# Kernel optimization log

Hardware: AMD Instinct MI355X
Metric: run time of the kernel (lower is better)

The kernel has to match this reference:

```python
import jax, jax.numpy as jnp
import numpy as np

N = 4096
F_IN = 512
ALPHA = 0.2          # LeakyReLU negative slope
NEG_INF = -9e15      # mask fill used by pyGAT


def setup_inputs() -> dict:
    key = jax.random.key(0)
    ks = jax.random.split(key, 9)
    x = jax.random.normal(ks[0], (N, F_IN), dtype=jnp.float32)
    adj = (jax.random.uniform(ks[1], (N, N)) < 0.005).astype(jnp.float32)
    adj = jnp.maximum(adj, jnp.eye(N, dtype=jnp.float32))
    s = 0.05
    W1 = jax.random.normal(ks[2], (512, 8, 128), dtype=jnp.float32) * s
    a_src1 = jax.random.normal(ks[3], (8, 128), dtype=jnp.float32) * s
    a_dst1 = jax.random.normal(ks[4], (8, 128), dtype=jnp.float32) * s
    W2 = jax.random.normal(ks[5], (1024, 1, 16), dtype=jnp.float32) * s
    a_src2 = jax.random.normal(ks[6], (1, 16), dtype=jnp.float32) * s
    a_dst2 = jax.random.normal(ks[7], (1, 16), dtype=jnp.float32) * s
    return {"x": x, "adj": adj, "W1": W1, "a_src1": a_src1, "a_dst1": a_dst1,
            "W2": W2, "a_src2": a_src2, "a_dst2": a_dst2}


def gat_layer(x, mask, W, a_src, a_dst, concat, activation):
    # x: [N, Fin], W: [Fin, H, Fout]
    h = jnp.einsum('nf,fho->nho', x, W)                  # [N, H, Fout]
    f_src = jnp.einsum('nho,ho->hn', h, a_src)            # [H, N]
    f_dst = jnp.einsum('nho,ho->hn', h, a_dst)            # [H, N]
    e = f_src[:, :, None] + f_dst[:, None, :]             # [H, N, N]
    e = jax.nn.leaky_relu(e, ALPHA)
    e = jnp.where(mask[None, :, :], e, NEG_INF)
    attn = jax.nn.softmax(e, axis=-1)                     # masked softmax over neighbors j
    out = jnp.einsum('hij,jho->iho', attn, h)             # [N, H, Fout]
    if concat:
        out = out.reshape(out.shape[0], -1)               # [N, H*Fout]
    else:
        out = out.mean(axis=1)                            # [N, Fout]
    if activation:
        out = jax.nn.elu(out)
    return out


def reference(x, adj, W1, a_src1, a_dst1, W2, a_src2, a_dst2):
    mask = adj > 0
    h1 = gat_layer(x, mask, W1, a_src1, a_dst1, concat=True, activation=True)
    h2 = gat_layer(h1, mask, W2, a_src2, a_dst2, concat=False, activation=False)
    out = jax.nn.elu(h2)
    return jax.nn.log_softmax(out, axis=1)
```

## Files before the change

### kernel.cpp

```cpp
#include <hip/hip_runtime.h>
#include <hip/hip_bf16.h>
#include <hip/hip_fp16.h>

typedef __attribute__((ext_vector_type(8))) short short8;
typedef __attribute__((ext_vector_type(8))) _Float16 half8;
typedef __attribute__((ext_vector_type(2))) _Float16 h2v;
typedef __attribute__((ext_vector_type(4))) float f32x4;
typedef __attribute__((ext_vector_type(2))) float f32x2;

#define MAXNBR 128
#define ALPHA 0.2f

static __device__ __forceinline__ unsigned short f2h(float f) {
    return __half_as_ushort(__float2half(f));
}
static __device__ __forceinline__ float h2f(unsigned short u) {
    return __half2float(__ushort_as_half(u));
}

__global__ __launch_bounds__(256) void cvt(const float* __restrict__ x,
                                           unsigned short* __restrict__ xh,
                                           const float* __restrict__ W1,
                                           unsigned short* __restrict__ W1t) {
    __shared__ float tile[64][65];
    int b = blockIdx.x, t = threadIdx.x;
    if (b < 1024) {
        size_t base = (size_t)b * 2048 + t * 8;
        float4 v0 = *(const float4*)&x[base];
        float4 v1 = *(const float4*)&x[base + 4];
        short8 o;
        o[0] = f2h(v0.x); o[1] = f2h(v0.y); o[2] = f2h(v0.z); o[3] = f2h(v0.w);
        o[4] = f2h(v1.x); o[5] = f2h(v1.y); o[6] = f2h(v1.z); o[7] = f2h(v1.w);
        *(short8*)&xh[base] = o;
    } else {
        int tb = b - 1024;
        int tk = (tb >> 4) * 64, tc = (tb & 15) * 64;
        int g = t >> 6, cx = t & 63;
        #pragma unroll
        for (int r = 0; r < 16; ++r)
            tile[g * 16 + r][cx] = W1[(size_t)(tk + g * 16 + r) * 1024 + tc + cx];
        __syncthreads();
        #pragma unroll
        for (int r = 0; r < 16; ++r)
            W1t[(size_t)(tc + g * 16 + r) * 512 + tk + cx] = f2h(tile[cx][g * 16 + r]);
    }
}

__global__ __launch_bounds__(256) void gemm_scan(const unsigned short* __restrict__ A,
                                                 const unsigned short* __restrict__ Bt,
                                                 unsigned short* __restrict__ C,
                                                 const float* __restrict__ adj,
                                                 int* __restrict__ nbr_idx,
                                                 int* __restrict__ nbr_cnt) {
    __shared__ unsigned short Asm[128 * 64];
    __shared__ unsigned short Bsm[64 * 64];
    __shared__ int wsum[4];
    int b = blockIdx.x;
    int tid = threadIdx.x;
    if (b < 512) {
        int lane = tid & 63;
        int w = tid >> 6;
        int wr = w >> 1, wc = w & 1;
        int rowBase = (b & 31) * 128, colBase = (b >> 5) * 64;
        int lr = lane >> 3;
        int lcs = ((lane & 7) ^ lr) * 8;
        f32x4 acc[4][2] = {};
        for (int k0 = 0; k0 < 512; k0 += 64) {
            #pragma unroll
            for (int i = 0; i < 4; ++i) {
                int rA = i * 32 + w * 8;
                __builtin_amdgcn_global_load_lds(
                    (const __attribute__((address_space(1))) void*)&A[(size_t)(rowBase + rA + lr) * 512 + k0 + lcs],
                    (__attribute__((address_space(3))) void*)&Asm[rA * 64],
                    16, 0, 0);
            }
            #pragma unroll
            for (int i = 0; i < 2; ++i) {
                int rB = i * 32 + w * 8;
                __builtin_amdgcn_global_load_lds(
                    (const __attribute__((address_space(1))) void*)&Bt[(size_t)(colBase + rB + lr) * 512 + k0 + lcs],
                    (__attribute__((address_space(3))) void*)&Bsm[rB * 64],
                    16, 0, 0);
            }
            __syncthreads();
            #pragma unroll
            for (int kk = 0; kk < 64; kk += 32) {
                half8 af[4], bfv[2];
                int kf = kk + (lane >> 4) * 8;
                #pragma unroll
                for (int m = 0; m < 4; ++m) {
                    int R = wr * 64 + m * 16 + (lane & 15);
                    af[m] = *(const half8*)&Asm[R * 64 + (kf ^ ((R & 7) << 3))];
                }
                #pragma unroll
                for (int n = 0; n < 2; ++n) {
                    int R = wc * 32 + n * 16 + (lane & 15);
                    bfv[n] = *(const half8*)&Bsm[R * 64 + (kf ^ ((R & 7) << 3))];
                }
                #pragma unroll
                for (int m = 0; m < 4; ++m)
                    #pragma unroll
                    for (int n = 0; n < 2; ++n)
                        acc[m][n] = __builtin_amdgcn_mfma_f32_16x16x32_f16(af[m], bfv[n], acc[m][n], 0, 0, 0);
            }
            __syncthreads();
        }
        int crow0 = rowBase + wr * 64, ccol0 = colBase + wc * 32;
        #pragma unroll
        for (int m = 0; m < 4; ++m)
            #pragma unroll
            for (int n = 0; n < 2; ++n) {
                int col = ccol0 + n * 16 + (lane & 15);
                int row0 = crow0 + m * 16 + (lane >> 4) * 4;
                #pragma unroll
                for (int r = 0; r < 4; ++r)
                    C[(size_t)(row0 + r) * 1024 + col] = f2h(acc[m][n][r]);
            }
    } else {
        int row = b - 512;
        int t = tid;
        const float* arow = adj + (size_t)row * 4096;
        const float4* ap = (const float4*)(arow + t * 16);
        float4 v0 = ap[0], v1 = ap[1], v2 = ap[2], v3 = ap[3];
        unsigned mask = 0;
        #pragma unroll
        for (int q = 0; q < 4; ++q) {
            if (((const float*)&v0)[q] > 0.f) mask |= 1u << q;
            if (((const float*)&v1)[q] > 0.f) mask |= 1u << (4 + q);
            if (((const float*)&v2)[q] > 0.f) mask |= 1u << (8 + q);
            if (((const float*)&v3)[q] > 0.f) mask |= 1u << (12 + q);
        }
        int mycnt = __popc(mask);
        int lane = t & 63, w = t >> 6;
        int incl = mycnt;
        #pragma unroll
        for (int d = 1; d < 64; d <<= 1) {
            int nn = __shfl_up(incl, d);
            if (lane >= d) incl += nn;
        }
        if (lane == 63) wsum[w] = incl;
        __syncthreads();
        int base = (w > 0 ? wsum[0] : 0) + (w > 1 ? wsum[1] : 0) + (w > 2 ? wsum[2] : 0);
        int pos = base + incl - mycnt;
        #pragma unroll
        for (int q = 0; q < 16; ++q) {
            if (mask & (1u << q)) {
                if (pos < MAXNBR) nbr_idx[row * MAXNBR + pos] = t * 16 + q;
                ++pos;
            }
        }
        if (t == 255) {
            int tot = base + incl;
            nbr_cnt[row] = tot < MAXNBR ? tot : MAXNBR;
        }
    }
}

__global__ __launch_bounds__(256) void attn_coef1(const unsigned short* __restrict__ h1h,
                                                  const float* __restrict__ a_src,
                                                  const float* __restrict__ a_dst,
                                                  float* __restrict__ fsp,
                                                  float* __restrict__ fdp,
                                                  unsigned char* __restrict__ h1q) {
    int n = blockIdx.x, t = threadIdx.x;
    ushort4 v = *(const ushort4*)&h1h[(size_t)n * 1024 + t * 4];
    int head = t >> 5;
    int o0 = (t * 4) & 127;
    float hv0 = h2f(v.x), hv1 = h2f(v.y), hv2 = h2f(v.z), hv3 = h2f(v.w);
    {
        int w8 = __builtin_amdgcn_cvt_pk_fp8_f32(hv0, hv1, 0, false);
        w8 = __builtin_amdgcn_cvt_pk_fp8_f32(hv2, hv3, w8, true);
        *(unsigned*)&h1q[(size_t)n * 1024 + t * 4] = (unsigned)w8;
    }
    float ps = hv0 * a_src[head * 128 + o0] + hv1 * a_src[head * 128 + o0 + 1]
             + hv2 * a_src[head * 128 + o0 + 2] + hv3 * a_src[head * 128 + o0 + 3];
    float pd = hv0 * a_dst[head * 128 + o0] + hv1 * a_dst[head * 128 + o0 + 1]
             + hv2 * a_dst[head * 128 + o0 + 2] + hv3 * a_dst[head * 128 + o0 + 3];
    #pragma unroll
    for (int off = 1; off < 32; off <<= 1) {
        ps += __shfl_xor(ps, off);
        pd += __shfl_xor(pd, off);
    }
    if ((t & 31) == 0) {
        fsp[n * 8 + head] = ps;
        fdp[n * 8 + head] = pd;
    }
}

__global__ __launch_bounds__(512) void aggregate7(const unsigned char* __restrict__ h1q,
                                                  const int* __restrict__ nbr_idx,
                                                  const int* __restrict__ nbr_cnt,
                                                  const float* __restrict__ fsp,
                                                  const float* __restrict__ fdp,
                                                  unsigned short* __restrict__ h1act) {
    __shared__ int nbr[MAXNBR];
    __shared__ float e_s[8][MAXNBR];
    __shared__ _Float16 attwS[8][MAXNBR];
    __shared__ half8 partS[3][128];
    int i = blockIdx.x;
    int t = threadIdx.x;
    int cnt = nbr_cnt[i];
    if (t < MAXNBR) {
        int nb = (t < cnt) ? nbr_idx[i * MAXNBR + t] : 0;
        nbr[t] = nb;
        if (t < cnt) {
            float4 fs0 = *(const float4*)&fsp[i * 8];
            float4 fs1 = *(const float4*)&fsp[i * 8 + 4];
            float4 d0 = *(const float4*)&fdp[nb * 8];
            float4 d1 = *(const float4*)&fdp[nb * 8 + 4];
            float e0 = fs0.x + d0.x, e1 = fs0.y + d0.y, e2 = fs0.z + d0.z, e3 = fs0.w + d0.w;
            float e4 = fs1.x + d1.x, e5 = fs1.y + d1.y, e6 = fs1.z + d1.z, e7 = fs1.w + d1.w;
            e_s[0][t] = e0 > 0.f ? e0 : ALPHA * e0;
            e_s[1][t] = e1 > 0.f ? e1 : ALPHA * e1;
            e_s[2][t] = e2 > 0.f ? e2 : ALPHA * e2;
            e_s[3][t] = e3 > 0.f ? e3 : ALPHA * e3;
            e_s[4][t] = e4 > 0.f ? e4 : ALPHA * e4;
            e_s[5][t] = e5 > 0.f ? e5 : ALPHA * e5;
            e_s[6][t] = e6 > 0.f ? e6 : ALPHA * e6;
            e_s[7][t] = e7 > 0.f ? e7 : ALPHA * e7;
        } else {
            #pragma unroll
            for (int h = 0; h < 8; ++h) e_s[h][t] = -INFINITY;
        }
    }
    __syncthreads();
    if (t < 256) {
        int h = t >> 5, sl = t & 31;
        float e[4];
        #pragma unroll
        for (int p = 0; p < 4; ++p) e[p] = e_s[h][sl + p * 32];
        float m = fmaxf(fmaxf(e[0], e[1]), fmaxf(e[2], e[3]));
        #pragma unroll
        for (int off = 1; off < 32; off <<= 1) m = fmaxf(m, __shfl_xor(m, off));
        float wq[4], s = 0.f;
        #pragma unroll
        for (int p = 0; p < 4; ++p) {
            wq[p] = (e[p] == -INFINITY) ? 0.f : __expf(e[p] - m);
            s += wq[p];
        }
        #pragma unroll
        for (int off = 1; off < 32; off <<= 1) s += __shfl_xor(s, off);
        float inv = 1.f / s;
        #pragma unroll
        for (int p = 0; p < 4; ++p)
            attwS[h][sl + p * 32] = (_Float16)(wq[p] * inv);
    }
    __syncthreads();
    int tf = t & 127;
    int par = t >> 7;
    int head = tf >> 4;
    const unsigned char* src = h1q + tf * 8;
    float acc[8] = {0.f, 0.f, 0.f, 0.f, 0.f, 0.f, 0.f, 0.f};
    int cntPad = (cnt + 3) & ~3;
    for (int j = par; j < cntPad; j += 4) {
        int nb = nbr[j];
        float wv = (float)attwS[head][j];
        uint2 v = *(const uint2*)&src[(size_t)nb << 10];
        f32x2 p0 = __builtin_amdgcn_cvt_pk_f32_fp8((int)v.x, false);
        f32x2 p1 = __builtin_amdgcn_cvt_pk_f32_fp8((int)v.x, true);
        f32x2 p2 = __builtin_amdgcn_cvt_pk_f32_fp8((int)v.y, false);
        f32x2 p3 = __builtin_amdgcn_cvt_pk_f32_fp8((int)v.y, true);
        acc[0] += wv * p0[0]; acc[1] += wv * p0[1];
        acc[2] += wv * p1[0]; acc[3] += wv * p1[1];
        acc[4] += wv * p2[0]; acc[5] += wv * p2[1];
        acc[6] += wv * p3[0]; acc[7] += wv * p3[1];
    }
    if (par > 0) {
        half8 st;
        #pragma unroll
        for (int q = 0; q < 8; ++q) st[q] = (_Float16)acc[q];
        partS[par - 1][tf] = st;
    }
    __syncthreads();
    if (par == 0) {
        half8 p0 = partS[0][tf], p1 = partS[1][tf], p2 = partS[2][tf];
        short8 o;
        #pragma unroll
        for (int q = 0; q < 8; ++q) {
            float a = acc[q] + (float)p0[q] + (float)p1[q] + (float)p2[q];
            a = a > 0.f ? a : (__expf(a) - 1.f);
            o[q] = f2h(a);
        }
        *(short8*)&h1act[(size_t)i * 1024 + tf * 8] = o;
    }
}

__global__ __launch_bounds__(256) void layer2_mfma(const unsigned short* __restrict__ h1act,
                                                   const float* __restrict__ W2,
                                                   const float* __restrict__ a_src2,
                                                   const float* __restrict__ a_dst2,
                                                   float* __restrict__ h2,
                                                   float2* __restrict__ fsd2) {
    __shared__ unsigned short W2t[16 * 1032];
    __shared__ float pred[4][256];
    int t = threadIdx.x, lane = t & 63, w = t >> 6;
    int rowBase = blockIdx.x * 16;
    for (int idx = t; idx < 16384; idx += 256) {
        int k = idx >> 4, o = idx & 15;
        W2t[o * 1032 + k] = f2h(W2[idx]);
    }
    __syncthreads();
    f32x4 acc = {};
    int r0 = lane & 15, kg = (lane >> 4) * 8;
    #pragma unroll
    for (int kk = 0; kk < 256; kk += 32) {
        int k0 = w * 256 + kk;
        half8 af = *(const half8*)&h1act[(size_t)(rowBase + r0) * 1024 + k0 + kg];
        half8 bf = *(const half8*)&W2t[r0 * 1032 + k0 + kg];
        acc = __builtin_amdgcn_mfma_f32_16x16x32_f16(af, bf, acc, 0, 0, 0);
    }
    #pragma unroll
    for (int r = 0; r < 4; ++r)
        pred[w][((lane >> 4) * 4 + r) * 16 + (lane & 15)] = acc[r];
    __syncthreads();
    if (t < 256) {
        int row = t >> 4, col = t & 15;
        float s = pred[0][t] + pred[1][t] + pred[2][t] + pred[3][t];
        h2[(rowBase + row) * 16 + col] = s;
        float ps = s * a_src2[col];
        float pd = s * a_dst2[col];
        #pragma unroll
        for (int off = 1; off < 16; off <<= 1) {
            ps += __shfl_xor(ps, off);
            pd += __shfl_xor(pd, off);
        }
        if (col == 0) fsd2[rowBase + row] = make_float2(ps, pd);
    }
}

__global__ __launch_bounds__(64) void final_layer(const float* __restrict__ h2,
                                                  const int* __restrict__ nbr_idx,
                                                  const int* __restrict__ nbr_cnt,
                                                  const float2* __restrict__ fsd2,
                                                  float* __restrict__ out) {
    __shared__ float attn[MAXNBR];
    __shared__ int nbr[MAXNBR];
    int i = blockIdx.x;
    int l = threadIdx.x;
    int cnt = nbr_cnt[i];
    float fsi = fsd2[i].x;
    for (int j = l; j < MAXNBR; j += 64) {
        float e = -INFINITY;
        if (j < cnt) {
            int jj = nbr_idx[i * MAXNBR + j];
            nbr[j] = jj;
            float xv = fsi + fsd2[jj].y;
            e = xv > 0.f ? xv : ALPHA * xv;
        }
        attn[j] = e;
    }
    __syncthreads();
    float m = fmaxf(attn[l], attn[l + 64]);
    #pragma unroll
    for (int off = 1; off < 64; off <<= 1) m = fmaxf(m, __shfl_xor(m, off));
    float s = 0.f;
    {
        float e0 = attn[l], e1 = attn[l + 64];
        if (e0 != -INFINITY) s += __expf(e0 - m);
        if (e1 != -INFINITY) s += __expf(e1 - m);
    }
    #pragma unroll
    for (int off = 1; off < 64; off <<= 1) s += __shfl_xor(s, off);
    for (int j = l; j < MAXNBR; j += 64) {
        float e = attn[j];
        attn[j] = (e == -INFINITY) ? 0.f : __expf(e - m) / s;
    }
    __syncthreads();
    if (l < 16) {
        float acc = 0.f;
        for (int j = 0; j < cnt; ++j)
            acc += attn[j] * h2[nbr[j] * 16 + l];
        float v = acc > 0.f ? acc : expm1f(acc);
        float mx = v;
        #pragma unroll
        for (int off = 1; off < 16; off <<= 1) mx = fmaxf(mx, __shfl_xor(mx, off));
        float se = __expf(v - mx);
        #pragma unroll
        for (int off = 1; off < 16; off <<= 1) se += __shfl_xor(se, off);
        out[i * 16 + l] = v - mx - logf(se);
    }
}

extern "C" void kernel_launch(void* const* d_in, const int* in_sizes, int n_in,
                              void* d_out, int out_size, void* d_ws, size_t ws_size,
                              hipStream_t stream) {
    const float* x      = (const float*)d_in[0];
    const float* adj    = (const float*)d_in[1];
    const float* W1     = (const float*)d_in[2];
    const float* a_src1 = (const float*)d_in[3];
    const float* a_dst1 = (const float*)d_in[4];
    const float* W2     = (const float*)d_in[5];
    const float* a_src2 = (const float*)d_in[6];
    const float* a_dst2 = (const float*)d_in[7];
    float* out = (float*)d_out;

    char* ws = (char*)d_ws;
    unsigned short* xh    = (unsigned short*)ws;
    unsigned short* w1t   = (unsigned short*)(ws + (4u << 20));
    unsigned short* h1h   = (unsigned short*)(ws + (6u << 20));
    float* fsp   = (float*)(ws + (14u << 20));
    float* fdp   = (float*)(ws + (14u << 20) + (128u << 10));
    float* h2    = (float*)(ws + (15u << 20));
    float2* fsd2 = (float2*)(ws + (15u << 20) + (256u << 10));
    int* nbr_idx = (int*)(ws + (16u << 20));
    int* nbr_cnt = (int*)(ws + (18u << 20));
    unsigned short* h1act = (unsigned short*)(ws + (26u << 20));
    unsigned char* h1q    = (unsigned char*)(ws + (34u << 20));

    cvt<<<1152, 256, 0, stream>>>(x, xh, W1, w1t);
    gemm_scan<<<4608, 256, 0, stream>>>(xh, w1t, h1h, adj, nbr_idx, nbr_cnt);
    attn_coef1<<<4096, 256, 0, stream>>>(h1h, a_src1, a_dst1, fsp, fdp, h1q);
    aggregate7<<<4096, 512, 0, stream>>>(h1q, nbr_idx, nbr_cnt, fsp, fdp, h1act);
    layer2_mfma<<<256, 256, 0, stream>>>(h1act, W2, a_src2, a_dst2, h2, fsd2);
    final_layer<<<4096, 64, 0, stream>>>(h2, nbr_idx, nbr_cnt, fsd2, out);
}
```

Measured before the change: 65.22 us.

## Fuse fp8 quantization into GEMM epilogue and pack multiple nodes per block

The GEMM epilogue now writes the fp8 copy of h1 directly, so the coefficient kernel no longer produces h1q and only computes the attention projections, with one wave per node and four nodes per block. The aggregation kernel handles two nodes per 512-thread block, each with 256 threads in two partitions instead of four. The final layer packs four nodes per block, drops its block barriers because each wave owns its own shared slices, and splits the neighbor sum across all 64 lanes. This cuts block count and launch overhead, but the epilogue now does scattered per-byte fp8 stores, which may be poorly coalesced.

```diff
diff --git a/kernel.cpp b/kernel.cpp
--- a/kernel.cpp
+++ b/kernel.cpp
@@ -4,7 +4,6 @@
 
 typedef __attribute__((ext_vector_type(8))) short short8;
 typedef __attribute__((ext_vector_type(8))) _Float16 half8;
-typedef __attribute__((ext_vector_type(2))) _Float16 h2v;
 typedef __attribute__((ext_vector_type(4))) float f32x4;
 typedef __attribute__((ext_vector_type(2))) float f32x2;
 
@@ -49,6 +48,7 @@
 __global__ __launch_bounds__(256) void gemm_scan(const unsigned short* __restrict__ A,
                                                  const unsigned short* __restrict__ Bt,
                                                  unsigned short* __restrict__ C,
+                                                 unsigned char* __restrict__ h1q,
                                                  const float* __restrict__ adj,
                                                  int* __restrict__ nbr_idx,
                                                  int* __restrict__ nbr_cnt) {
@@ -113,8 +113,12 @@
                 int col = ccol0 + n * 16 + (lane & 15);
                 int row0 = crow0 + m * 16 + (lane >> 4) * 4;
                 #pragma unroll
-                for (int r = 0; r < 4; ++r)
-                    C[(size_t)(row0 + r) * 1024 + col] = f2h(acc[m][n][r]);
+                for (int r = 0; r < 4; ++r) {
+                    float v = acc[m][n][r];
+                    C[(size_t)(row0 + r) * 1024 + col] = f2h(v);
+                    int w8 = __builtin_amdgcn_cvt_pk_fp8_f32(v, v, 0, false);
+                    h1q[(size_t)(row0 + r) * 1024 + col] = (unsigned char)w8;
+                }
             }
     } else {
         int row = b - 512;
@@ -156,79 +160,80 @@
     }
 }
 
-__global__ __launch_bounds__(256) void attn_coef1(const unsigned short* __restrict__ h1h,
+__global__ __launch_bounds__(256) void attn_coef2(const unsigned short* __restrict__ h1h,
                                                   const float* __restrict__ a_src,
                                                   const float* __restrict__ a_dst,
                                                   float* __restrict__ fsp,
-                                                  float* __restrict__ fdp,
-                                                  unsigned char* __restrict__ h1q) {
-    int n = blockIdx.x, t = threadIdx.x;
-    ushort4 v = *(const ushort4*)&h1h[(size_t)n * 1024 + t * 4];
-    int head = t >> 5;
-    int o0 = (t * 4) & 127;
-    float hv0 = h2f(v.x), hv1 = h2f(v.y), hv2 = h2f(v.z), hv3 = h2f(v.w);
-    {
-        int w8 = __builtin_amdgcn_cvt_pk_fp8_f32(hv0, hv1, 0, false);
-        w8 = __builtin_amdgcn_cvt_pk_fp8_f32(hv2, hv3, w8, true);
-        *(unsigned*)&h1q[(size_t)n * 1024 + t * 4] = (unsigned)w8;
-    }
-    float ps = hv0 * a_src[head * 128 + o0] + hv1 * a_src[head * 128 + o0 + 1]
-             + hv2 * a_src[head * 128 + o0 + 2] + hv3 * a_src[head * 128 + o0 + 3];
-    float pd = hv0 * a_dst[head * 128 + o0] + hv1 * a_dst[head * 128 + o0 + 1]
-             + hv2 * a_dst[head * 128 + o0 + 2] + hv3 * a_dst[head * 128 + o0 + 3];
-    #pragma unroll
-    for (int off = 1; off < 32; off <<= 1) {
-        ps += __shfl_xor(ps, off);
-        pd += __shfl_xor(pd, off);
-    }
-    if ((t & 31) == 0) {
+                                                  float* __restrict__ fdp) {
+    int t = threadIdx.x;
+    int n = blockIdx.x * 4 + (t >> 6);
+    int l = t & 63;
+    int head = l >> 3;
+    const unsigned short* src = h1h + (size_t)n * 1024 + l * 16;
+    const float* as = a_src + head * 128 + (l & 7) * 16;
+    const float* ad = a_dst + head * 128 + (l & 7) * 16;
+    float ps = 0.f, pd = 0.f;
+    #pragma unroll
+    for (int q = 0; q < 4; ++q) {
+        ushort4 v = *(const ushort4*)&src[q * 4];
+        float4 a4 = *(const float4*)&as[q * 4];
+        float4 d4 = *(const float4*)&ad[q * 4];
+        float h0 = h2f(v.x), h1 = h2f(v.y), h2_ = h2f(v.z), h3 = h2f(v.w);
+        ps += h0 * a4.x + h1 * a4.y + h2_ * a4.z + h3 * a4.w;
+        pd += h0 * d4.x + h1 * d4.y + h2_ * d4.z + h3 * d4.w;
+    }
+    ps += __shfl_xor(ps, 1); ps += __shfl_xor(ps, 2); ps += __shfl_xor(ps, 4);
+    pd += __shfl_xor(pd, 1); pd += __shfl_xor(pd, 2); pd += __shfl_xor(pd, 4);
+    if ((l & 7) == 0) {
         fsp[n * 8 + head] = ps;
         fdp[n * 8 + head] = pd;
     }
 }
 
-__global__ __launch_bounds__(512) void aggregate7(const unsigned char* __restrict__ h1q,
+__global__ __launch_bounds__(512) void aggregate8(const unsigned char* __restrict__ h1q,
                                                   const int* __restrict__ nbr_idx,
                                                   const int* __restrict__ nbr_cnt,
                                                   const float* __restrict__ fsp,
                                                   const float* __restrict__ fdp,
                                                   unsigned short* __restrict__ h1act) {
-    __shared__ int nbr[MAXNBR];
-    __shared__ float e_s[8][MAXNBR];
-    __shared__ _Float16 attwS[8][MAXNBR];
-    __shared__ half8 partS[3][128];
-    int i = blockIdx.x;
+    __shared__ int nbrS[2][MAXNBR];
+    __shared__ float e_s[2][8][MAXNBR];
+    __shared__ _Float16 attwS[2][8][MAXNBR];
+    __shared__ half8 partS[2][128];
     int t = threadIdx.x;
+    int sub = t >> 8, tl = t & 255;
+    int i = blockIdx.x * 2 + sub;
     int cnt = nbr_cnt[i];
-    if (t < MAXNBR) {
-        int nb = (t < cnt) ? nbr_idx[i * MAXNBR + t] : 0;
-        nbr[t] = nb;
-        if (t < cnt) {
+    int* nbr = nbrS[sub];
+    if (tl < MAXNBR) {
+        int nb = (tl < cnt) ? nbr_idx[i * MAXNBR + tl] : 0;
+        nbr[tl] = nb;
+        if (tl < cnt) {
             float4 fs0 = *(const float4*)&fsp[i * 8];
             float4 fs1 = *(const float4*)&fsp[i * 8 + 4];
             float4 d0 = *(const float4*)&fdp[nb * 8];
             float4 d1 = *(const float4*)&fdp[nb * 8 + 4];
             float e0 = fs0.x + d0.x, e1 = fs0.y + d0.y, e2 = fs0.z + d0.z, e3 = fs0.w + d0.w;
             float e4 = fs1.x + d1.x, e5 = fs1.y + d1.y, e6 = fs1.z + d1.z, e7 = fs1.w + d1.w;
-            e_s[0][t] = e0 > 0.f ? e0 : ALPHA * e0;
-            e_s[1][t] = e1 > 0.f ? e1 : ALPHA * e1;
-            e_s[2][t] = e2 > 0.f ? e2 : ALPHA * e2;
-            e_s[3][t] = e3 > 0.f ? e3 : ALPHA * e3;
-            e_s[4][t] = e4 > 0.f ? e4 : ALPHA * e4;
-            e_s[5][t] = e5 > 0.f ? e5 : ALPHA * e5;
-            e_s[6][t] = e6 > 0.f ? e6 : ALPHA * e6;
-            e_s[7][t] = e7 > 0.f ? e7 : ALPHA * e7;
+            e_s[sub][0][tl] = e0 > 0.f ? e0 : ALPHA * e0;
+            e_s[sub][1][tl] = e1 > 0.f ? e1 : ALPHA * e1;
+            e_s[sub][2][tl] = e2 > 0.f ? e2 : ALPHA * e2;
+            e_s[sub][3][tl] = e3 > 0.f ? e3 : ALPHA * e3;
+            e_s[sub][4][tl] = e4 > 0.f ? e4 : ALPHA * e4;
+            e_s[sub][5][tl] = e5 > 0.f ? e5 : ALPHA * e5;
+            e_s[sub][6][tl] = e6 > 0.f ? e6 : ALPHA * e6;
+            e_s[sub][7][tl] = e7 > 0.f ? e7 : ALPHA * e7;
         } else {
             #pragma unroll
-            for (int h = 0; h < 8; ++h) e_s[h][t] = -INFINITY;
+            for (int h = 0; h < 8; ++h) e_s[sub][h][tl] = -INFINITY;
         }
     }
     __syncthreads();
-    if (t < 256) {
-        int h = t >> 5, sl = t & 31;
+    {
+        int h = tl >> 5, sl = tl & 31;
         float e[4];
         #pragma unroll
-        for (int p = 0; p < 4; ++p) e[p] = e_s[h][sl + p * 32];
+        for (int p = 0; p < 4; ++p) e[p] = e_s[sub][h][sl + p * 32];
         float m = fmaxf(fmaxf(e[0], e[1]), fmaxf(e[2], e[3]));
         #pragma unroll
         for (int off = 1; off < 32; off <<= 1) m = fmaxf(m, __shfl_xor(m, off));
@@ -243,18 +248,18 @@
         float inv = 1.f / s;
         #pragma unroll
         for (int p = 0; p < 4; ++p)
-            attwS[h][sl + p * 32] = (_Float16)(wq[p] * inv);
+            attwS[sub][h][sl + p * 32] = (_Float16)(wq[p] * inv);
     }
     __syncthreads();
-    int tf = t & 127;
-    int par = t >> 7;
+    int tf = tl & 127;
+    int par = tl >> 7;
     int head = tf >> 4;
     const unsigned char* src = h1q + tf * 8;
     float acc[8] = {0.f, 0.f, 0.f, 0.f, 0.f, 0.f, 0.f, 0.f};
-    int cntPad = (cnt + 3) & ~3;
-    for (int j = par; j < cntPad; j += 4) {
+    int cntPad = (cnt + 1) & ~1;
+    for (int j = par; j < cntPad; j += 2) {
         int nb = nbr[j];
-        float wv = (float)attwS[head][j];
+        float wv = (float)attwS[sub][head][j];
         uint2 v = *(const uint2*)&src[(size_t)nb << 10];
         f32x2 p0 = __builtin_amdgcn_cvt_pk_f32_fp8((int)v.x, false);
         f32x2 p1 = __builtin_amdgcn_cvt_pk_f32_fp8((int)v.x, true);
@@ -265,19 +270,19 @@
         acc[4] += wv * p2[0]; acc[5] += wv * p2[1];
         acc[6] += wv * p3[0]; acc[7] += wv * p3[1];
     }
-    if (par > 0) {
+    if (par) {
         half8 st;
         #pragma unroll
         for (int q = 0; q < 8; ++q) st[q] = (_Float16)acc[q];
-        partS[par - 1][tf] = st;
+        partS[sub][tf] = st;
     }
     __syncthreads();
-    if (par == 0) {
-        half8 p0 = partS[0][tf], p1 = partS[1][tf], p2 = partS[2][tf];
+    if (!par) {
+        half8 p0 = partS[sub][tf];
         short8 o;
         #pragma unroll
         for (int q = 0; q < 8; ++q) {
-            float a = acc[q] + (float)p0[q] + (float)p1[q] + (float)p2[q];
+            float a = acc[q] + (float)p0[q];
             a = a > 0.f ? a : (__expf(a) - 1.f);
             o[q] = f2h(a);
         }
@@ -328,17 +333,21 @@
     }
 }
 
-__global__ __launch_bounds__(64) void final_layer(const float* __restrict__ h2,
-                                                  const int* __restrict__ nbr_idx,
-                                                  const int* __restrict__ nbr_cnt,
-                                                  const float2* __restrict__ fsd2,
-                                                  float* __restrict__ out) {
-    __shared__ float attn[MAXNBR];
-    __shared__ int nbr[MAXNBR];
-    int i = blockIdx.x;
-    int l = threadIdx.x;
+__global__ __launch_bounds__(256) void final_layer2(const float* __restrict__ h2,
+                                                    const int* __restrict__ nbr_idx,
+                                                    const int* __restrict__ nbr_cnt,
+                                                    const float2* __restrict__ fsd2,
+                                                    float* __restrict__ out) {
+    __shared__ float attnS[4][MAXNBR];
+    __shared__ int nbrS[4][MAXNBR];
+    int t = threadIdx.x;
+    int w = t >> 6, l = t & 63;
+    int i = blockIdx.x * 4 + w;
+    float* attn = attnS[w];
+    int* nbr = nbrS[w];
     int cnt = nbr_cnt[i];
     float fsi = fsd2[i].x;
+    #pragma unroll
     for (int j = l; j < MAXNBR; j += 64) {
         float e = -INFINITY;
         if (j < cnt) {
@@ -349,7 +358,6 @@
         }
         attn[j] = e;
     }
-    __syncthreads();
     float m = fmaxf(attn[l], attn[l + 64]);
     #pragma unroll
     for (int off = 1; off < 64; off <<= 1) m = fmaxf(m, __shfl_xor(m, off));
@@ -361,15 +369,18 @@
     }
     #pragma unroll
     for (int off = 1; off < 64; off <<= 1) s += __shfl_xor(s, off);
+    #pragma unroll
     for (int j = l; j < MAXNBR; j += 64) {
         float e = attn[j];
         attn[j] = (e == -INFINITY) ? 0.f : __expf(e - m) / s;
     }
-    __syncthreads();
+    int o = l & 15, p = l >> 4;
+    float acc = 0.f;
+    for (int j = p; j < cnt; j += 4)
+        acc += attn[j] * h2[nbr[j] * 16 + o];
+    acc += __shfl_xor(acc, 16);
+    acc += __shfl_xor(acc, 32);
     if (l < 16) {
-        float acc = 0.f;
-        for (int j = 0; j < cnt; ++j)
-            acc += attn[j] * h2[nbr[j] * 16 + l];
         float v = acc > 0.f ? acc : expm1f(acc);
         float mx = v;
         #pragma unroll
@@ -408,9 +419,9 @@
     unsigned char* h1q    = (unsigned char*)(ws + (34u << 20));
 
     cvt<<<1152, 256, 0, stream>>>(x, xh, W1, w1t);
-    gemm_scan<<<4608, 256, 0, stream>>>(xh, w1t, h1h, adj, nbr_idx, nbr_cnt);
-    attn_coef1<<<4096, 256, 0, stream>>>(h1h, a_src1, a_dst1, fsp, fdp, h1q);
-    aggregate7<<<4096, 512, 0, stream>>>(h1q, nbr_idx, nbr_cnt, fsp, fdp, h1act);
+    gemm_scan<<<4608, 256, 0, stream>>>(xh, w1t, h1h, h1q, adj, nbr_idx, nbr_cnt);
+    attn_coef2<<<1024, 256, 0, stream>>>(h1h, a_src1, a_dst1, fsp, fdp);
+    aggregate8<<<2048, 512, 0, stream>>>(h1q, nbr_idx, nbr_cnt, fsp, fdp, h1act);
     layer2_mfma<<<256, 256, 0, stream>>>(h1act, W2, a_src2, a_dst2, h2, fsd2);
-    final_layer<<<4096, 64, 0, stream>>>(h2, nbr_idx, nbr_cnt, fsd2, out);
-}
+    final_layer2<<<1024, 256, 0, stream>>>(h2, nbr_idx, nbr_cnt, fsd2, out);
+}
```

New measurement: 64.35 us (median of 2 runs). No clear change (-1.3%).
